# Optimization experiments

Hardware: AMD Instinct MI355X
Metric: run time of the kernel (lower is better)

Reference implementation:

```python
import jax, jax.numpy as jnp
import numpy as np

N = 100000
E = 3200000
IN_DIM = 128
HID = 64
BN_EPS = 1e-5


def _gcn_conv(x, W, b, src, dst, dinv):
    h = x @ W                                      # [N, out]
    coeff = (dinv[src] * dinv[dst])[:, None]       # [E, 1]
    msg = h[src] * coeff                           # gather over edges
    agg = jax.ops.segment_sum(msg, dst, num_segments=N)
    agg = agg + h * (dinv * dinv)[:, None]         # self-loop term
    return agg + b


def setup_inputs() -> dict:
    key = jax.random.key(0)
    ks = jax.random.split(key, 12)
    x = jax.random.normal(ks[0], (N, IN_DIM), dtype=jnp.float32)
    edge_index = jax.random.randint(ks[1], (2, E), 0, N, dtype=jnp.int64)
    s1 = 1.0 / np.sqrt(IN_DIM)
    s2 = 1.0 / np.sqrt(HID)
    W1 = jax.random.uniform(ks[2], (IN_DIM, HID), jnp.float32, -s1, s1)
    b1 = jnp.zeros((HID,), jnp.float32)
    W2 = jax.random.uniform(ks[3], (HID, HID), jnp.float32, -s2, s2)
    b2 = jnp.zeros((HID,), jnp.float32)
    W3 = jax.random.uniform(ks[4], (HID, 1), jnp.float32, -s2, s2)
    b3 = jnp.zeros((1,), jnp.float32)
    g1 = jnp.ones((HID,), jnp.float32)
    beta1 = jnp.zeros((HID,), jnp.float32)
    m1 = 0.1 * jax.random.normal(ks[5], (HID,), jnp.float32)
    v1 = jax.random.uniform(ks[6], (HID,), jnp.float32) + 0.5
    g2 = jnp.ones((HID,), jnp.float32)
    beta2 = jnp.zeros((HID,), jnp.float32)
    m2 = 0.1 * jax.random.normal(ks[7], (HID,), jnp.float32)
    v2 = jax.random.uniform(ks[8], (HID,), jnp.float32) + 0.5
    return {"x": x, "edge_index": edge_index,
            "W1": W1, "b1": b1, "W2": W2, "b2": b2, "W3": W3, "b3": b3,
            "g1": g1, "beta1": beta1, "m1": m1, "v1": v1,
            "g2": g2, "beta2": beta2, "m2": m2, "v2": v2}


def reference(x, edge_index, W1, b1, W2, b2, W3, b3,
              g1, beta1, m1, v1, g2, beta2, m2, v2):
    src, dst = edge_index[0], edge_index[1]
    # degree with self-loops (computed on destination index, PyG convention)
    deg = jax.ops.segment_sum(jnp.ones((E,), jnp.float32), dst, num_segments=N) + 1.0
    dinv = jax.lax.rsqrt(deg)

    def bn(h, g, beta, m, v):
        return (h - m) * jax.lax.rsqrt(v + BN_EPS) * g + beta

    h = _gcn_conv(x, W1, b1, src, dst, dinv)
    h = jax.nn.relu(bn(h, g1, beta1, m1, v1))  # dropout is a no-op in eval
    h = _gcn_conv(h, W2, b2, src, dst, dinv)
    h = jax.nn.relu(bn(h, g2, beta2, m2, v2))
    h = _gcn_conv(h, W3, b3, src, dst, dinv)
    return jax.nn.sigmoid(h)  # [N, 1]
```

## Files before the change

### kernel.cpp

```cpp
#include <hip/hip_runtime.h>
#include <math.h>

#define N_NODES 100000
#define E_EDGES 3200000
#define IN_DIM_ 128
#define HID_ 64
#define BN_EPS_ 1e-5f

#define PB 200
#define CHUNK 16000
#define NBUCK 391
#define BMAX 9600

typedef __attribute__((ext_vector_type(8))) short short8;
typedef __attribute__((ext_vector_type(4))) float f32x4;

__device__ inline ushort f2bf(float f) {
    union { float f; unsigned u; } c; c.f = f;
    unsigned r = c.u + 0x7fff + ((c.u >> 16) & 1);
    return (ushort)(r >> 16);
}
__device__ inline float bf_lo(unsigned p) { union { unsigned u; float f; } c; c.u = p << 16; return c.f; }
__device__ inline float bf_hi(unsigned p) { union { unsigned u; float f; } c; c.u = p & 0xffff0000u; return c.f; }

__global__ __launch_bounds__(256) void passA1_hist(const int* __restrict__ ei,
                                                   int* __restrict__ histPB) {
    __shared__ int hist[NBUCK];
    int t = threadIdx.x, b = blockIdx.x;
    for (int k = t; k < NBUCK; k += 256) hist[k] = 0;
    __syncthreads();
    int e0 = b * CHUNK, e1 = e0 + CHUNK;
    for (int e = e0 + t; e < e1; e += 256) {
        int d = ei[E_EDGES + e];
        atomicAdd(&hist[d >> 8], 1);
    }
    __syncthreads();
    for (int k = t; k < NBUCK; k += 256) histPB[k * PB + b] = hist[k];
}

__global__ __launch_bounds__(256) void scan_rows(int* __restrict__ histPB,
                                                 int* __restrict__ bucket_tot) {
    __shared__ int wsum[4];
    int k = blockIdx.x, t = threadIdx.x, lane = t & 63, wv = t >> 6;
    int v = (t < PB) ? histPB[k * PB + t] : 0;
    int s = v;
#pragma unroll
    for (int off = 1; off < 64; off <<= 1) {
        int u = __shfl_up(s, off, 64);
        if (lane >= off) s += u;
    }
    if (lane == 63) wsum[wv] = s;
    __syncthreads();
    int wbase = 0;
    for (int w = 0; w < wv; w++) wbase += wsum[w];
    if (t < PB) histPB[k * PB + t] = wbase + s - v;
    if (t == 255) bucket_tot[k] = wbase + s;
}

__global__ __launch_bounds__(512) void scan_totals(const int* __restrict__ bucket_tot,
                                                   int* __restrict__ bucket_base,
                                                   int* __restrict__ row_ptr) {
    __shared__ int wsum[8];
    int t = threadIdx.x, lane = t & 63, wv = t >> 6;
    int v = (t < NBUCK) ? bucket_tot[t] : 0;
    int s = v;
#pragma unroll
    for (int off = 1; off < 64; off <<= 1) {
        int u = __shfl_up(s, off, 64);
        if (lane >= off) s += u;
    }
    if (lane == 63) wsum[wv] = s;
    __syncthreads();
    int wbase = 0;
    for (int w = 0; w < wv; w++) wbase += wsum[w];
    if (t < NBUCK) bucket_base[t] = wbase + s - v;
    if (t == 0) {
        bucket_base[NBUCK] = E_EDGES;
        row_ptr[N_NODES] = E_EDGES;
    }
}

__global__ __launch_bounds__(256) void passA2_sorted(const int* __restrict__ ei,
                                                     const int* __restrict__ histPB,
                                                     const int* __restrict__ bucket_base,
                                                     int* __restrict__ ebuf) {
    __shared__ int sorted[CHUNK];
    __shared__ ushort bid[CHUNK];
    __shared__ int cur[NBUCK];
    __shared__ int lbase[NBUCK];
    int t = threadIdx.x, b = blockIdx.x;
    for (int k = t; k < NBUCK; k += 256) cur[k] = 0;
    __syncthreads();
    int e0 = b * CHUNK;
    for (int e = e0 + t; e < e0 + CHUNK; e += 256)
        atomicAdd(&cur[ei[E_EDGES + e] >> 8], 1);
    __syncthreads();
    if (t < 64) {
        int run = 0;
        for (int c0 = 0; c0 < NBUCK; c0 += 64) {
            int idx = c0 + t;
            int v = (idx < NBUCK) ? cur[idx] : 0;
            int s = v;
#pragma unroll
            for (int off = 1; off < 64; off <<= 1) {
                int u = __shfl_up(s, off, 64);
                if (t >= off) s += u;
            }
            if (idx < NBUCK) lbase[idx] = run + s - v;
            run += __shfl(s, 63, 64);
        }
    }
    __syncthreads();
    for (int k = t; k < NBUCK; k += 256) cur[k] = lbase[k];
    __syncthreads();
    for (int e = e0 + t; e < e0 + CHUNK; e += 256) {
        int s = ei[e];
        int d = ei[E_EDGES + e];
        int k = d >> 8;
        int pos = atomicAdd(&cur[k], 1);
        sorted[pos] = s | ((d & 255) << 17);
        bid[pos] = (ushort)k;
    }
    __syncthreads();
    for (int j = t; j < CHUNK; j += 256) {
        int k = bid[j];
        int dest = bucket_base[k] + histPB[k * PB + b] + (j - lbase[k]);
        ebuf[dest] = sorted[j];
    }
}

__global__ __launch_bounds__(256) void passB_sorted(const int* __restrict__ ebuf,
                                                    const int* __restrict__ bucket_base,
                                                    int* __restrict__ row_ptr,
                                                    int* __restrict__ csr_src,
                                                    float* __restrict__ dinv) {
    __shared__ int sorted[BMAX];
    __shared__ int hist[256];
    __shared__ int wsum[4];
    int b = blockIdx.x, t = threadIdx.x, lane = t & 63, wv = t >> 6;
    int base = bucket_base[b], end = bucket_base[b + 1];
    hist[t] = 0;
    __syncthreads();
    for (int k = base + t; k < end; k += 256)
        atomicAdd(&hist[ebuf[k] >> 17], 1);
    __syncthreads();
    int v = hist[t];
    int s = v;
#pragma unroll
    for (int off = 1; off < 64; off <<= 1) {
        int u = __shfl_up(s, off, 64);
        if (lane >= off) s += u;
    }
    if (lane == 63) wsum[wv] = s;
    __syncthreads();
    int wbase = 0;
    for (int w = 0; w < wv; w++) wbase += wsum[w];
    int excl = wbase + s - v;
    int node = b * 256 + t;
    if (node < N_NODES) {
        row_ptr[node] = base + excl;
        dinv[node] = rsqrtf((float)v + 1.0f);
    }
    __syncthreads();
    hist[t] = excl;
    __syncthreads();
    for (int k = base + t; k < end; k += 256) {
        int pv = ebuf[k];
        int pos = atomicAdd(&hist[pv >> 17], 1);
        if (pos < BMAX) sorted[pos] = pv;
        else csr_src[base + pos] = pv & 0x1FFFF;
    }
    __syncthreads();
    int cnt = end - base;
    if (cnt > BMAX) cnt = BMAX;
    for (int j = t; j < cnt; j += 256)
        csr_src[base + j] = sorted[j] & 0x1FFFF;
}

template<int K, bool BF16IN>
__global__ __launch_bounds__(256) void gemm_bf16(const void* __restrict__ Xv,
                                                 const float* __restrict__ W,
                                                 const float* __restrict__ dinv,
                                                 ushort* __restrict__ hs) {
    constexpr int KP = K + 8;
    __shared__ ushort A_lds[64][KP];
    __shared__ ushort Wt_lds[64][KP];
    int t = threadIdx.x;
    long row0 = (long)blockIdx.x * 64;

    for (int i = t; i < K * 16; i += 256) {
        float4 w4 = ((const float4*)W)[i];
        int k = i >> 4, n = (i & 15) * 4;
        Wt_lds[n + 0][k] = f2bf(w4.x);
        Wt_lds[n + 1][k] = f2bf(w4.y);
        Wt_lds[n + 2][k] = f2bf(w4.z);
        Wt_lds[n + 3][k] = f2bf(w4.w);
    }
    if (BF16IN) {
        constexpr int K2 = K / 2;
        const unsigned* X = (const unsigned*)Xv;
        for (int i = t; i < 64 * K2; i += 256) {
            int r = i / K2, c = i % K2;
            unsigned val = 0;
            long row = row0 + r;
            if (row < N_NODES) val = X[row * K2 + c];
            *(unsigned*)&A_lds[r][c * 2] = val;
        }
    } else {
        constexpr int K4 = K / 4;
        const float* X = (const float*)Xv;
        for (int i = t; i < 64 * K4; i += 256) {
            int r = i / K4, c = i % K4;
            float4 val = make_float4(0.f, 0.f, 0.f, 0.f);
            long row = row0 + r;
            if (row < N_NODES) val = ((const float4*)X)[row * K4 + c];
            int cb = c * 4;
            A_lds[r][cb + 0] = f2bf(val.x);
            A_lds[r][cb + 1] = f2bf(val.y);
            A_lds[r][cb + 2] = f2bf(val.z);
            A_lds[r][cb + 3] = f2bf(val.w);
        }
    }
    __syncthreads();

    int w = t >> 6, l = t & 63;
    int m = l & 15, quad = l >> 4;
    f32x4 acc[4];
#pragma unroll
    for (int c = 0; c < 4; c++) acc[c] = (f32x4){0.f, 0.f, 0.f, 0.f};

#pragma unroll
    for (int ch = 0; ch < K / 32; ch++) {
        short8 a = *(const short8*)&A_lds[16 * w + m][32 * ch + 8 * quad];
#pragma unroll
        for (int c = 0; c < 4; c++) {
            short8 b = *(const short8*)&Wt_lds[16 * c + m][32 * ch + 8 * quad];
            acc[c] = __builtin_amdgcn_mfma_f32_16x16x32_bf16(a, b, acc[c], 0, 0, 0);
        }
    }

#pragma unroll
    for (int r = 0; r < 4; r++) {
        long node = row0 + 16 * w + quad * 4 + r;
        if (node < N_NODES) {
            float dv = dinv[node];
#pragma unroll
            for (int c = 0; c < 4; c++)
                hs[node * 64 + 16 * c + m] = f2bf(acc[c][r] * dv);
        }
    }
}

template<bool LAST>
__global__ __launch_bounds__(256) void gather_feat(const int* __restrict__ row_ptr,
                                                   const int* __restrict__ csr_src,
                                                   const ushort* __restrict__ hs,
                                                   const float* __restrict__ dinv,
                                                   const float* __restrict__ b,
                                                   const float* __restrict__ g,
                                                   const float* __restrict__ beta,
                                                   const float* __restrict__ m,
                                                   const float* __restrict__ v,
                                                   unsigned* __restrict__ y,
                                                   const float* __restrict__ W3,
                                                   float* __restrict__ hs3, int n) {
    int i = (blockIdx.x * 256 + threadIdx.x) >> 6;
    if (i >= n) return;
    int l = threadIdx.x & 63;
    int es = l >> 3, fg = l & 7;
    const uint4* H4 = (const uint4*)hs;

    float a0 = 0.f, a1 = 0.f, a2 = 0.f, a3 = 0.f;
    float a4 = 0.f, a5 = 0.f, a6 = 0.f, a7 = 0.f;

    if (es == 0) {
        uint4 p = H4[(long)i * 8 + fg];
        a0 += bf_lo(p.x); a1 += bf_hi(p.x);
        a2 += bf_lo(p.y); a3 += bf_hi(p.y);
        a4 += bf_lo(p.z); a5 += bf_hi(p.z);
        a6 += bf_lo(p.w); a7 += bf_hi(p.w);
    }

    int beg = row_ptr[i], end = row_ptr[i + 1];
    int k = beg;
    for (; k + 16 <= end; k += 16) {
        int sA = csr_src[k + es];
        int sB = csr_src[k + 8 + es];
        uint4 pA = H4[(long)sA * 8 + fg];
        uint4 pB = H4[(long)sB * 8 + fg];
        a0 += bf_lo(pA.x) + bf_lo(pB.x); a1 += bf_hi(pA.x) + bf_hi(pB.x);
        a2 += bf_lo(pA.y) + bf_lo(pB.y); a3 += bf_hi(pA.y) + bf_hi(pB.y);
        a4 += bf_lo(pA.z) + bf_lo(pB.z); a5 += bf_hi(pA.z) + bf_hi(pB.z);
        a6 += bf_lo(pA.w) + bf_lo(pB.w); a7 += bf_hi(pA.w) + bf_hi(pB.w);
    }
    for (; k + 8 <= end; k += 8) {
        int s = csr_src[k + es];
        uint4 p = H4[(long)s * 8 + fg];
        a0 += bf_lo(p.x); a1 += bf_hi(p.x);
        a2 += bf_lo(p.y); a3 += bf_hi(p.y);
        a4 += bf_lo(p.z); a5 += bf_hi(p.z);
        a6 += bf_lo(p.w); a7 += bf_hi(p.w);
    }
    int rem = end - k;
    if (es < rem) {
        int s = csr_src[k + es];
        uint4 p = H4[(long)s * 8 + fg];
        a0 += bf_lo(p.x); a1 += bf_hi(p.x);
        a2 += bf_lo(p.y); a3 += bf_hi(p.y);
        a4 += bf_lo(p.z); a5 += bf_hi(p.z);
        a6 += bf_lo(p.w); a7 += bf_hi(p.w);
    }

#pragma unroll
    for (int off = 8; off < 64; off <<= 1) {
        a0 += __shfl_xor(a0, off, 64);
        a1 += __shfl_xor(a1, off, 64);
        a2 += __shfl_xor(a2, off, 64);
        a3 += __shfl_xor(a3, off, 64);
        a4 += __shfl_xor(a4, off, 64);
        a5 += __shfl_xor(a5, off, 64);
        a6 += __shfl_xor(a6, off, 64);
        a7 += __shfl_xor(a7, off, 64);
    }

    float4 bb0 = ((const float4*)b)[fg * 2],    bb1 = ((const float4*)b)[fg * 2 + 1];
    float4 gg0 = ((const float4*)g)[fg * 2],    gg1 = ((const float4*)g)[fg * 2 + 1];
    float4 be0 = ((const float4*)beta)[fg * 2], be1 = ((const float4*)beta)[fg * 2 + 1];
    float4 mm0 = ((const float4*)m)[fg * 2],    mm1 = ((const float4*)m)[fg * 2 + 1];
    float4 vv0 = ((const float4*)v)[fg * 2],    vv1 = ((const float4*)v)[fg * 2 + 1];
    float di = dinv[i];
    float o0 = fmaxf((di * a0 + bb0.x - mm0.x) * (gg0.x * rsqrtf(vv0.x + BN_EPS_)) + be0.x, 0.f);
    float o1 = fmaxf((di * a1 + bb0.y - mm0.y) * (gg0.y * rsqrtf(vv0.y + BN_EPS_)) + be0.y, 0.f);
    float o2 = fmaxf((di * a2 + bb0.z - mm0.z) * (gg0.z * rsqrtf(vv0.z + BN_EPS_)) + be0.z, 0.f);
    float o3 = fmaxf((di * a3 + bb0.w - mm0.w) * (gg0.w * rsqrtf(vv0.w + BN_EPS_)) + be0.w, 0.f);
    float o4 = fmaxf((di * a4 + bb1.x - mm1.x) * (gg1.x * rsqrtf(vv1.x + BN_EPS_)) + be1.x, 0.f);
    float o5 = fmaxf((di * a5 + bb1.y - mm1.y) * (gg1.y * rsqrtf(vv1.y + BN_EPS_)) + be1.y, 0.f);
    float o6 = fmaxf((di * a6 + bb1.z - mm1.z) * (gg1.z * rsqrtf(vv1.z + BN_EPS_)) + be1.z, 0.f);
    float o7 = fmaxf((di * a7 + bb1.w - mm1.w) * (gg1.w * rsqrtf(vv1.w + BN_EPS_)) + be1.w, 0.f);

    if (LAST) {
        float4 w30 = ((const float4*)W3)[fg * 2], w31 = ((const float4*)W3)[fg * 2 + 1];
        float p = o0 * w30.x + o1 * w30.y + o2 * w30.z + o3 * w30.w +
                  o4 * w31.x + o5 * w31.y + o6 * w31.z + o7 * w31.w;
#pragma unroll
        for (int off = 1; off < 8; off <<= 1)
            p += __shfl_xor(p, off, 64);
        if (l == 0) hs3[i] = p * di;
    } else {
        if (es == 0) {
            uint4 pk;
            pk.x = (unsigned)f2bf(o0) | ((unsigned)f2bf(o1) << 16);
            pk.y = (unsigned)f2bf(o2) | ((unsigned)f2bf(o3) << 16);
            pk.z = (unsigned)f2bf(o4) | ((unsigned)f2bf(o5) << 16);
            pk.w = (unsigned)f2bf(o6) | ((unsigned)f2bf(o7) << 16);
            ((uint4*)y)[(long)i * 8 + fg] = pk;
        }
    }
}

__global__ __launch_bounds__(256) void gather3(const int* __restrict__ row_ptr,
                                               const int* __restrict__ csr_src,
                                               const float* __restrict__ hs3,
                                               const float* __restrict__ dinv,
                                               const float* __restrict__ b3,
                                               float* __restrict__ out, int n) {
    int i = blockIdx.x * 256 + threadIdx.x;
    if (i >= n) return;
    int beg = row_ptr[i], end = row_ptr[i + 1];
    float s0 = hs3[i], s1 = 0.f, s2 = 0.f, s3 = 0.f;
    float s4 = 0.f, s5 = 0.f, s6 = 0.f, s7 = 0.f;
    int k = beg;
    for (; k + 8 <= end; k += 8) {
        s0 += hs3[csr_src[k]];
        s1 += hs3[csr_src[k + 1]];
        s2 += hs3[csr_src[k + 2]];
        s3 += hs3[csr_src[k + 3]];
        s4 += hs3[csr_src[k + 4]];
        s5 += hs3[csr_src[k + 5]];
        s6 += hs3[csr_src[k + 6]];
        s7 += hs3[csr_src[k + 7]];
    }
    for (; k < end; k++) s0 += hs3[csr_src[k]];
    float z = dinv[i] * (((s0 + s1) + (s2 + s3)) + ((s4 + s5) + (s6 + s7))) + b3[0];
    out[i] = 1.f / (1.f + expf(-z));
}

extern "C" void kernel_launch(void* const* d_in, const int* in_sizes, int n_in,
                              void* d_out, int out_size, void* d_ws, size_t ws_size,
                              hipStream_t stream) {
    const int N = N_NODES;
    const int E = E_EDGES;

    const float* x   = (const float*)d_in[0];
    const int*   ei  = (const int*)d_in[1];
    const float* W1  = (const float*)d_in[2];
    const float* b1  = (const float*)d_in[3];
    const float* W2  = (const float*)d_in[4];
    const float* b2  = (const float*)d_in[5];
    const float* W3  = (const float*)d_in[6];
    const float* b3  = (const float*)d_in[7];
    const float* g1  = (const float*)d_in[8];
    const float* bt1 = (const float*)d_in[9];
    const float* m1  = (const float*)d_in[10];
    const float* v1  = (const float*)d_in[11];
    const float* g2  = (const float*)d_in[12];
    const float* bt2 = (const float*)d_in[13];
    const float* m2  = (const float*)d_in[14];
    const float* v2  = (const float*)d_in[15];
    float* out = (float*)d_out;

    int*    wsi         = (int*)d_ws;
    float*  dinv        = (float*)wsi;
    float*  hs3         = (float*)(wsi + (long)N);
    int*    row_ptr     = wsi + 2L * N;
    int*    histPB      = wsi + 3L * N + 16;
    int*    bucket_tot  = histPB + NBUCK * PB;
    int*    bucket_base = bucket_tot + 400;
    int*    csr_src     = bucket_base + 400;
    ushort* hsb         = (ushort*)(csr_src + (long)E);
    unsigned* yb        = (unsigned*)(csr_src + (long)E + 32L * N);
    int*    ebuf        = (int*)hsb;

    passA1_hist<<<PB, 256, 0, stream>>>(ei, histPB);
    scan_rows<<<NBUCK, 256, 0, stream>>>(histPB, bucket_tot);
    scan_totals<<<1, 512, 0, stream>>>(bucket_tot, bucket_base, row_ptr);
    passA2_sorted<<<PB, 256, 0, stream>>>(ei, histPB, bucket_base, ebuf);
    passB_sorted<<<NBUCK, 256, 0, stream>>>(ebuf, bucket_base, row_ptr, csr_src, dinv);

    gemm_bf16<IN_DIM_, false><<<(N + 63) / 64, 256, 0, stream>>>(x, W1, dinv, hsb);
    gather_feat<false><<<N / 4, 256, 0, stream>>>(row_ptr, csr_src, hsb, dinv,
                                                  b1, g1, bt1, m1, v1, yb, W3, hs3, N);
    gemm_bf16<HID_, true><<<(N + 63) / 64, 256, 0, stream>>>(yb, W2, dinv, hsb);
    gather_feat<true><<<N / 4, 256, 0, stream>>>(row_ptr, csr_src, hsb, dinv,
                                                 b2, g2, bt2, m2, v2, yb, W3, hs3, N);
    gather3<<<(N + 255) / 256, 256, 0, stream>>>(row_ptr, csr_src, hs3, dinv, b3, out, N);
}
```

Before: 433.4 us.

## Unroll gather with zero-row padding, packed bf16 unpack, and wider sort blocks

The neighbour gather loop now issues four independent row loads per iteration, one edge slot per lane group. Out-of-range slots point to an extra all-zero row at index N, which the GEMM writes by scaling with dinv=0. Addressing uses 32-bit byte offsets, and bf16 pairs are unpacked into packed float2 adds. The aim is more loads in flight and fewer instructions per edge, at the cost of some wasted loads on short rows. Separately, the edge-sorting passes use 250 blocks of 512 threads with smaller chunks instead of 200 blocks of 256 threads.

```diff
diff --git a/kernel.cpp b/kernel.cpp
--- a/kernel.cpp
+++ b/kernel.cpp
@@ -7,13 +7,14 @@
 #define HID_ 64
 #define BN_EPS_ 1e-5f
 
-#define PB 200
-#define CHUNK 16000
+#define PB 250
+#define CHUNK 12800
 #define NBUCK 391
 #define BMAX 9600
 
 typedef __attribute__((ext_vector_type(8))) short short8;
 typedef __attribute__((ext_vector_type(4))) float f32x4;
+typedef __attribute__((ext_vector_type(2))) float f32x2;
 
 __device__ inline ushort f2bf(float f) {
     union { float f; unsigned u; } c; c.f = f;
@@ -22,20 +23,25 @@
 }
 __device__ inline float bf_lo(unsigned p) { union { unsigned u; float f; } c; c.u = p << 16; return c.f; }
 __device__ inline float bf_hi(unsigned p) { union { unsigned u; float f; } c; c.u = p & 0xffff0000u; return c.f; }
-
-__global__ __launch_bounds__(256) void passA1_hist(const int* __restrict__ ei,
+__device__ inline f32x2 up2(unsigned u) {
+    union { unsigned u; float f; } lo, hi;
+    lo.u = u << 16; hi.u = u & 0xffff0000u;
+    f32x2 r; r.x = lo.f; r.y = hi.f; return r;
+}
+
+__global__ __launch_bounds__(512) void passA1_hist(const int* __restrict__ ei,
                                                    int* __restrict__ histPB) {
     __shared__ int hist[NBUCK];
     int t = threadIdx.x, b = blockIdx.x;
-    for (int k = t; k < NBUCK; k += 256) hist[k] = 0;
+    for (int k = t; k < NBUCK; k += 512) hist[k] = 0;
     __syncthreads();
     int e0 = b * CHUNK, e1 = e0 + CHUNK;
-    for (int e = e0 + t; e < e1; e += 256) {
+    for (int e = e0 + t; e < e1; e += 512) {
         int d = ei[E_EDGES + e];
         atomicAdd(&hist[d >> 8], 1);
     }
     __syncthreads();
-    for (int k = t; k < NBUCK; k += 256) histPB[k * PB + b] = hist[k];
+    for (int k = t; k < NBUCK; k += 512) histPB[k * PB + b] = hist[k];
 }
 
 __global__ __launch_bounds__(256) void scan_rows(int* __restrict__ histPB,
@@ -80,7 +86,7 @@
     }
 }
 
-__global__ __launch_bounds__(256) void passA2_sorted(const int* __restrict__ ei,
+__global__ __launch_bounds__(512) void passA2_sorted(const int* __restrict__ ei,
                                                      const int* __restrict__ histPB,
                                                      const int* __restrict__ bucket_base,
                                                      int* __restrict__ ebuf) {
@@ -89,10 +95,10 @@
     __shared__ int cur[NBUCK];
     __shared__ int lbase[NBUCK];
     int t = threadIdx.x, b = blockIdx.x;
-    for (int k = t; k < NBUCK; k += 256) cur[k] = 0;
+    for (int k = t; k < NBUCK; k += 512) cur[k] = 0;
     __syncthreads();
     int e0 = b * CHUNK;
-    for (int e = e0 + t; e < e0 + CHUNK; e += 256)
+    for (int e = e0 + t; e < e0 + CHUNK; e += 512)
         atomicAdd(&cur[ei[E_EDGES + e] >> 8], 1);
     __syncthreads();
     if (t < 64) {
@@ -111,9 +117,9 @@
         }
     }
     __syncthreads();
-    for (int k = t; k < NBUCK; k += 256) cur[k] = lbase[k];
-    __syncthreads();
-    for (int e = e0 + t; e < e0 + CHUNK; e += 256) {
+    for (int k = t; k < NBUCK; k += 512) cur[k] = lbase[k];
+    __syncthreads();
+    for (int e = e0 + t; e < e0 + CHUNK; e += 512) {
         int s = ei[e];
         int d = ei[E_EDGES + e];
         int k = d >> 8;
@@ -122,7 +128,7 @@
         bid[pos] = (ushort)k;
     }
     __syncthreads();
-    for (int j = t; j < CHUNK; j += 256) {
+    for (int j = t; j < CHUNK; j += 512) {
         int k = bid[j];
         int dest = bucket_base[k] + histPB[k * PB + b] + (j - lbase[k]);
         ebuf[dest] = sorted[j];
@@ -242,8 +248,8 @@
 #pragma unroll
     for (int r = 0; r < 4; r++) {
         long node = row0 + 16 * w + quad * 4 + r;
-        if (node < N_NODES) {
-            float dv = dinv[node];
+        if (node <= N_NODES) {
+            float dv = (node < N_NODES) ? dinv[node] : 0.f;
 #pragma unroll
             for (int c = 0; c < 4; c++)
                 hs[node * 64 + 16 * c + m] = f2bf(acc[c][r] * dv);
@@ -268,48 +274,41 @@
     if (i >= n) return;
     int l = threadIdx.x & 63;
     int es = l >> 3, fg = l & 7;
-    const uint4* H4 = (const uint4*)hs;
-
-    float a0 = 0.f, a1 = 0.f, a2 = 0.f, a3 = 0.f;
-    float a4 = 0.f, a5 = 0.f, a6 = 0.f, a7 = 0.f;
+    const char* Hb = (const char*)hs;
+    unsigned foff = (unsigned)fg << 4;
+    unsigned zoff = ((unsigned)N_NODES << 7) + foff;
+
+    f32x2 a01 = {0.f, 0.f}, a23 = {0.f, 0.f}, a45 = {0.f, 0.f}, a67 = {0.f, 0.f};
 
     if (es == 0) {
-        uint4 p = H4[(long)i * 8 + fg];
-        a0 += bf_lo(p.x); a1 += bf_hi(p.x);
-        a2 += bf_lo(p.y); a3 += bf_hi(p.y);
-        a4 += bf_lo(p.z); a5 += bf_hi(p.z);
-        a6 += bf_lo(p.w); a7 += bf_hi(p.w);
+        uint4 p = *(const uint4*)(Hb + (((unsigned)i << 7) + foff));
+        a01 += up2(p.x); a23 += up2(p.y); a45 += up2(p.z); a67 += up2(p.w);
     }
 
     int beg = row_ptr[i], end = row_ptr[i + 1];
-    int k = beg;
-    for (; k + 16 <= end; k += 16) {
-        int sA = csr_src[k + es];
-        int sB = csr_src[k + 8 + es];
-        uint4 pA = H4[(long)sA * 8 + fg];
-        uint4 pB = H4[(long)sB * 8 + fg];
-        a0 += bf_lo(pA.x) + bf_lo(pB.x); a1 += bf_hi(pA.x) + bf_hi(pB.x);
-        a2 += bf_lo(pA.y) + bf_lo(pB.y); a3 += bf_hi(pA.y) + bf_hi(pB.y);
-        a4 += bf_lo(pA.z) + bf_lo(pB.z); a5 += bf_hi(pA.z) + bf_hi(pB.z);
-        a6 += bf_lo(pA.w) + bf_lo(pB.w); a7 += bf_hi(pA.w) + bf_hi(pB.w);
-    }
-    for (; k + 8 <= end; k += 8) {
-        int s = csr_src[k + es];
-        uint4 p = H4[(long)s * 8 + fg];
-        a0 += bf_lo(p.x); a1 += bf_hi(p.x);
-        a2 += bf_lo(p.y); a3 += bf_hi(p.y);
-        a4 += bf_lo(p.z); a5 += bf_hi(p.z);
-        a6 += bf_lo(p.w); a7 += bf_hi(p.w);
-    }
-    int rem = end - k;
-    if (es < rem) {
-        int s = csr_src[k + es];
-        uint4 p = H4[(long)s * 8 + fg];
-        a0 += bf_lo(p.x); a1 += bf_hi(p.x);
-        a2 += bf_lo(p.y); a3 += bf_hi(p.y);
-        a4 += bf_lo(p.z); a5 += bf_hi(p.z);
-        a6 += bf_lo(p.w); a7 += bf_hi(p.w);
-    }
+    int endm1 = end - 1;
+    for (int k = beg + es; k < end; k += 32) {
+        int c1 = k + 8, c2 = k + 16, c3 = k + 24;
+        int s0 = csr_src[k];
+        int s1 = csr_src[c1 < end ? c1 : endm1];
+        int s2 = csr_src[c2 < end ? c2 : endm1];
+        int s3 = csr_src[c3 < end ? c3 : endm1];
+        unsigned o0 = ((unsigned)s0 << 7) + foff;
+        unsigned o1 = (c1 < end) ? (((unsigned)s1 << 7) + foff) : zoff;
+        unsigned o2 = (c2 < end) ? (((unsigned)s2 << 7) + foff) : zoff;
+        unsigned o3 = (c3 < end) ? (((unsigned)s3 << 7) + foff) : zoff;
+        uint4 p0 = *(const uint4*)(Hb + o0);
+        uint4 p1 = *(const uint4*)(Hb + o1);
+        uint4 p2 = *(const uint4*)(Hb + o2);
+        uint4 p3 = *(const uint4*)(Hb + o3);
+        a01 += up2(p0.x); a23 += up2(p0.y); a45 += up2(p0.z); a67 += up2(p0.w);
+        a01 += up2(p1.x); a23 += up2(p1.y); a45 += up2(p1.z); a67 += up2(p1.w);
+        a01 += up2(p2.x); a23 += up2(p2.y); a45 += up2(p2.z); a67 += up2(p2.w);
+        a01 += up2(p3.x); a23 += up2(p3.y); a45 += up2(p3.z); a67 += up2(p3.w);
+    }
+
+    float a0 = a01.x, a1 = a01.y, a2 = a23.x, a3 = a23.y;
+    float a4 = a45.x, a5 = a45.y, a6 = a67.x, a7 = a67.y;
 
 #pragma unroll
     for (int off = 8; off < 64; off <<= 1) {
@@ -418,13 +417,13 @@
     int*    bucket_base = bucket_tot + 400;
     int*    csr_src     = bucket_base + 400;
     ushort* hsb         = (ushort*)(csr_src + (long)E);
-    unsigned* yb        = (unsigned*)(csr_src + (long)E + 32L * N);
+    unsigned* yb        = (unsigned*)(csr_src + (long)E + 32L * (N + 1));
     int*    ebuf        = (int*)hsb;
 
-    passA1_hist<<<PB, 256, 0, stream>>>(ei, histPB);
+    passA1_hist<<<PB, 512, 0, stream>>>(ei, histPB);
     scan_rows<<<NBUCK, 256, 0, stream>>>(histPB, bucket_tot);
     scan_totals<<<1, 512, 0, stream>>>(bucket_tot, bucket_base, row_ptr);
-    passA2_sorted<<<PB, 256, 0, stream>>>(ei, histPB, bucket_base, ebuf);
+    passA2_sorted<<<PB, 512, 0, stream>>>(ei, histPB, bucket_base, ebuf);
     passB_sorted<<<NBUCK, 256, 0, stream>>>(ebuf, bucket_base, row_ptr, csr_src, dinv);
 
     gemm_bf16<IN_DIM_, false><<<(N + 63) / 64, 256, 0, stream>>>(x, W1, dinv, hsb);
```

New measurement: 397.5 us. -8.3%, faster.
